# Performance work log

Measured on AMD Instinct MI355X. Metric: run time of the kernel, lower is better.

Reference implementation:

```python
import jax, jax.numpy as jnp
import numpy as np

IMG = 224                      # hardcoded image_size in apply_mask
K = int(0.25 * IMG * IMG)      # 12544 pixels masked per sample


def setup_inputs() -> dict:
    key = jax.random.key(0)
    k1, k2 = jax.random.split(key)
    B = 256
    data = jax.random.normal(k1, (B, IMG, IMG, 3), dtype=jnp.float32)
    # |gradients| flattened over (H, W, C) -> length IMG*IMG*3, nonnegative
    line_grad = jax.random.uniform(k2, (B, IMG * IMG * 3), dtype=jnp.float32)
    return {"data": data, "line_grad": line_grad}


def _mask_one(d, g):
    # d: [IMG, IMG, 3], g: [IMG*IMG*3]
    _, idx = jax.lax.top_k(g, K)              # flat indices into (H,W,C)
    reduced = jnp.mod(idx, IMG * IMG)         # fold channel offset -> spatial
    rows = reduced // IMG
    cols = reduced % IMG
    # scatter zeros across all 3 channels at the selected pixels
    return d.at[rows, cols].set(0.0)


def reference(data, line_grad):
    # vectorized_map over the batch -> vmap
    return jax.vmap(_mask_one)(data, line_grad)
```

## Files before the change

### kernel.cpp

```cpp
#include <hip/hip_runtime.h>

#define IMG    224
#define NPIX   (IMG * IMG)
#define NELEM  (NPIX * 3)
#define KSEL   12544
#define NBINS  4096
#define MAXCAND 2048
#define NMASKW (NPIX / 32)
#define NVEC   (NELEM / 4)
#define BLOCK  1024

__global__ __launch_bounds__(BLOCK) void masked_model_kernel(
    const float* __restrict__ data,
    const float* __restrict__ grad,
    float* __restrict__ out)
{
    const int b   = blockIdx.x;
    const int tid = threadIdx.x;

    const float* g = grad + (size_t)b * NELEM;
    const float* d = data + (size_t)b * NELEM;
    float*       o = out  + (size_t)b * NELEM;

    __shared__ unsigned int hist[NBINS];
    __shared__ unsigned int suffixP[BLOCK + 1];
    __shared__ unsigned int mask[NMASKW];
    __shared__ unsigned int candkey[MAXCAND];
    __shared__ unsigned int candidx[MAXCAND];
    __shared__ unsigned int candcnt;
    __shared__ int sB1;
    __shared__ unsigned int sR;

    for (int i = tid; i < NBINS; i += BLOCK) hist[i] = 0u;
    for (int i = tid; i < NMASKW; i += BLOCK) mask[i] = 0u;
    if (tid == 0) { candcnt = 0u; suffixP[BLOCK] = 0u; }
    __syncthreads();

    const float4* g4 = (const float4*)g;
    for (int i = tid; i < NVEC; i += BLOCK) {
        float4 v = g4[i];
        int b0 = min((int)(v.x * 4096.0f), NBINS - 1);
        int b1 = min((int)(v.y * 4096.0f), NBINS - 1);
        int b2 = min((int)(v.z * 4096.0f), NBINS - 1);
        int b3 = min((int)(v.w * 4096.0f), NBINS - 1);
        atomicAdd(&hist[b0], 1u);
        atomicAdd(&hist[b1], 1u);
        atomicAdd(&hist[b2], 1u);
        atomicAdd(&hist[b3], 1u);
    }
    __syncthreads();

    {
        unsigned int s = hist[4 * tid] + hist[4 * tid + 1]
                       + hist[4 * tid + 2] + hist[4 * tid + 3];
        suffixP[tid] = s;
        __syncthreads();
        for (int off = 1; off < BLOCK; off <<= 1) {
            unsigned int v = suffixP[tid];
            if (tid + off < BLOCK) v += suffixP[tid + off];
            __syncthreads();
            suffixP[tid] = v;
            __syncthreads();
        }
    }

    {
        unsigned int a  = suffixP[tid];
        unsigned int nx = suffixP[tid + 1];
        if (a >= KSEL && nx < KSEL) {
            unsigned int cum = nx;
            for (int i = 3; i >= 0; --i) {
                unsigned int h = hist[4 * tid + i];
                cum += h;
                if (cum >= KSEL) {
                    sB1 = 4 * tid + i;
                    sR  = KSEL - (cum - h);
                    break;
                }
            }
        }
    }
    __syncthreads();

    {
        const int B1 = sB1;
        for (int i = tid; i < NVEC; i += BLOCK) {
            float4 v = g4[i];
            int base = 4 * i;
            float vv[4] = {v.x, v.y, v.z, v.w};
            #pragma unroll
            for (int c = 0; c < 4; ++c) {
                int bin = min((int)(vv[c] * 4096.0f), NBINS - 1);
                if (bin > B1) {
                    int idx = base + c;
                    int p = idx % NPIX;
                    atomicOr(&mask[p >> 5], 1u << (p & 31));
                } else if (bin == B1) {
                    unsigned int c2 = atomicAdd(&candcnt, 1u);
                    if (c2 < MAXCAND) {
                        candkey[c2] = __float_as_uint(vv[c]);
                        candidx[c2] = (unsigned int)(base + c);
                    }
                }
            }
        }
    }
    __syncthreads();

    {
        unsigned int n = candcnt < MAXCAND ? candcnt : MAXCAND;
        unsigned int r = sR;
        for (unsigned int j = tid; j < n; j += BLOCK) {
            unsigned int kj = candkey[j];
            unsigned int ij = candidx[j];
            unsigned int rank = 0;
            for (unsigned int i = 0; i < n; ++i) {
                unsigned int ki = candkey[i];
                rank += (ki > kj) || (ki == kj && candidx[i] < ij);
            }
            if (rank < r) {
                int p = (int)(ij % NPIX);
                atomicOr(&mask[p >> 5], 1u << (p & 31));
            }
        }
    }
    __syncthreads();

    {
        const float4* d4 = (const float4*)d;
        float4*       o4 = (float4*)o;
        for (int i = tid; i < NVEC; i += BLOCK) {
            float4 v = d4[i];
            int e = 4 * i;
            int p0 = e / 3, p1 = (e + 1) / 3, p2 = (e + 2) / 3, p3 = (e + 3) / 3;
            if ((mask[p0 >> 5] >> (p0 & 31)) & 1u) v.x = 0.0f;
            if ((mask[p1 >> 5] >> (p1 & 31)) & 1u) v.y = 0.0f;
            if ((mask[p2 >> 5] >> (p2 & 31)) & 1u) v.z = 0.0f;
            if ((mask[p3 >> 5] >> (p3 & 31)) & 1u) v.w = 0.0f;
            o4[i] = v;
        }
    }
}

extern "C" void kernel_launch(void* const* d_in, const int* in_sizes, int n_in,
                              void* d_out, int out_size, void* d_ws, size_t ws_size,
                              hipStream_t stream) {
    const float* data = (const float*)d_in[0];
    const float* grad = (const float*)d_in[1];
    float* out = (float*)d_out;

    const int B = in_sizes[0] / NELEM;
    masked_model_kernel<<<B, BLOCK, 0, stream>>>(data, grad, out);
}
```

Before: 386.2 us.

## Split per-sample top-k masking into multi-kernel pipeline with more blocks per sample

Replaces the single block-per-sample kernel with four kernels: a chunked histogram built in workspace, a wave-shuffle suffix scan to find the threshold bin, a per-pixel-chunk apply kernel that checks all three channel planes per pixel and collects boundary candidates, and a small tie-resolution kernel that zeroes the extra pixels in the output. The aim is more parallelism than 256 large blocks allow, and removing the serial Hillis-Steele scan. In exchange it adds extra launches, a memset and reads the gradients twice from global memory. The candidate cap drops to 512, and the old kernel is used only when the workspace is too small.

New measurement: 397.3 us. 1.03x slower.

```diff
diff --git a/kernel.cpp b/kernel.cpp
--- a/kernel.cpp
+++ b/kernel.cpp
@@ -5,9 +5,185 @@
 #define NELEM  (NPIX * 3)
 #define KSEL   12544
 #define NBINS  4096
+#define NVEC4  (NELEM / 4)
+
+#define K1_CHUNKS 4
+#define K1_BLOCK  256
+#define K1_V4     (NVEC4 / K1_CHUNKS)
+
+#define CH        8
+#define PIX_PER   (NPIX / CH)
+#define QUADS_PER (PIX_PER / 4)
+#define MWORDS    (PIX_PER / 32)
+#define EV4_PER   (PIX_PER * 3 / 4)
+
+#define CAP 512
+
+__global__ __launch_bounds__(K1_BLOCK) void k1_hist(
+    const float* __restrict__ grad, unsigned int* __restrict__ hist)
+{
+    const int s     = blockIdx.x >> 2;
+    const int chunk = blockIdx.x & 3;
+    const float4* g4 = (const float4*)(grad + (size_t)s * NELEM);
+
+    __shared__ unsigned int h[NBINS];
+    for (int i = threadIdx.x; i < NBINS; i += K1_BLOCK) h[i] = 0u;
+    __syncthreads();
+
+    const int beg = chunk * K1_V4, end = beg + K1_V4;
+    for (int i = beg + threadIdx.x; i < end; i += K1_BLOCK) {
+        float4 v = g4[i];
+        atomicAdd(&h[min((int)(v.x * 4096.0f), NBINS - 1)], 1u);
+        atomicAdd(&h[min((int)(v.y * 4096.0f), NBINS - 1)], 1u);
+        atomicAdd(&h[min((int)(v.z * 4096.0f), NBINS - 1)], 1u);
+        atomicAdd(&h[min((int)(v.w * 4096.0f), NBINS - 1)], 1u);
+    }
+    __syncthreads();
+
+    unsigned int* gh = hist + (size_t)s * NBINS;
+    for (int i = threadIdx.x; i < NBINS; i += K1_BLOCK)
+        if (h[i]) atomicAdd(&gh[i], h[i]);
+}
+
+__global__ __launch_bounds__(1024) void k2_scan(
+    const unsigned int* __restrict__ hist,
+    uint2* __restrict__ thr, unsigned int* __restrict__ candcnt)
+{
+    const int s   = blockIdx.x;
+    const int tid = threadIdx.x;
+    const unsigned int* h = hist + (size_t)s * NBINS;
+
+    unsigned int h0 = h[4 * tid], h1 = h[4 * tid + 1];
+    unsigned int h2 = h[4 * tid + 2], h3 = h[4 * tid + 3];
+    const unsigned int gsum = h0 + h1 + h2 + h3;
+
+    const int lane = tid & 63, w = tid >> 6;
+    unsigned int v = gsum;
+    #pragma unroll
+    for (int off = 1; off < 64; off <<= 1) {
+        unsigned int u = __shfl_down(v, off, 64);
+        if (lane + off < 64) v += u;
+    }
+    __shared__ unsigned int wtot[16];
+    if (lane == 0) wtot[w] = v;
+    __syncthreads();
+    unsigned int tail = 0;
+    for (int i = w + 1; i < 16; ++i) tail += wtot[i];
+
+    const unsigned int suffix     = v + tail;
+    const unsigned int suffixNext = suffix - gsum;
+
+    if (suffix >= KSEL && suffixNext < KSEL) {
+        unsigned int cum = suffixNext;
+        unsigned int hh[4] = {h0, h1, h2, h3};
+        for (int i = 3; i >= 0; --i) {
+            cum += hh[i];
+            if (cum >= KSEL) {
+                thr[s] = make_uint2((unsigned)(4 * tid + i),
+                                    (unsigned)(KSEL - (cum - hh[i])));
+                break;
+            }
+        }
+    }
+    if (tid == 0) candcnt[s] = 0u;
+}
+
+__global__ __launch_bounds__(256) void k3_apply(
+    const float* __restrict__ data, const float* __restrict__ grad,
+    const uint2* __restrict__ thr,
+    unsigned int* __restrict__ candcnt,
+    unsigned int* __restrict__ candkey, unsigned int* __restrict__ candidx,
+    float* __restrict__ out)
+{
+    const int s     = blockIdx.x >> 3;
+    const int chunk = blockIdx.x & 7;
+    const int p0    = chunk * PIX_PER;
+
+    const uint2 t  = thr[s];
+    const float t0 = (float)t.x * (1.0f / 4096.0f);
+    const float t1 = (float)(t.x + 1) * (1.0f / 4096.0f);
+
+    __shared__ unsigned int mask[MWORDS];
+    for (int i = threadIdx.x; i < MWORDS; i += 256) mask[i] = 0u;
+    __syncthreads();
+
+    const float4* g4 = (const float4*)(grad + (size_t)s * NELEM);
+    unsigned int* ck = candkey + (size_t)s * CAP;
+    unsigned int* ci = candidx + (size_t)s * CAP;
+
+    for (int q = threadIdx.x; q < QUADS_PER; q += 256) {
+        const int p = p0 + 4 * q;
+        float4 a = g4[p >> 2];
+        float4 b = g4[(p + NPIX) >> 2];
+        float4 c = g4[(p + 2 * NPIX) >> 2];
+        float av[4] = {a.x, a.y, a.z, a.w};
+        float bv[4] = {b.x, b.y, b.z, b.w};
+        float cv[4] = {c.x, c.y, c.z, c.w};
+        unsigned int m = 0;
+        #pragma unroll
+        for (int j = 0; j < 4; ++j) {
+            if ((av[j] >= t1) || (bv[j] >= t1) || (cv[j] >= t1)) m |= (1u << j);
+            if (av[j] >= t0 && av[j] < t1) {
+                unsigned int cc = atomicAdd(&candcnt[s], 1u);
+                if (cc < CAP) { ck[cc] = __float_as_uint(av[j]); ci[cc] = (unsigned)(p + j); }
+            }
+            if (bv[j] >= t0 && bv[j] < t1) {
+                unsigned int cc = atomicAdd(&candcnt[s], 1u);
+                if (cc < CAP) { ck[cc] = __float_as_uint(bv[j]); ci[cc] = (unsigned)(NPIX + p + j); }
+            }
+            if (cv[j] >= t0 && cv[j] < t1) {
+                unsigned int cc = atomicAdd(&candcnt[s], 1u);
+                if (cc < CAP) { ck[cc] = __float_as_uint(cv[j]); ci[cc] = (unsigned)(2 * NPIX + p + j); }
+            }
+        }
+        if (m) atomicOr(&mask[q >> 3], m << ((4 * q) & 31));
+    }
+    __syncthreads();
+
+    const float4* d4 = (const float4*)(data + (size_t)s * NELEM + (size_t)3 * p0);
+    float4*       o4 = (float4*)(out  + (size_t)s * NELEM + (size_t)3 * p0);
+    for (int i = threadIdx.x; i < EV4_PER; i += 256) {
+        float4 v = d4[i];
+        const int e = 4 * i;
+        const int lp0 = e / 3, lp1 = (e + 1) / 3, lp2 = (e + 2) / 3, lp3 = (e + 3) / 3;
+        if ((mask[lp0 >> 5] >> (lp0 & 31)) & 1u) v.x = 0.0f;
+        if ((mask[lp1 >> 5] >> (lp1 & 31)) & 1u) v.y = 0.0f;
+        if ((mask[lp2 >> 5] >> (lp2 & 31)) & 1u) v.z = 0.0f;
+        if ((mask[lp3 >> 5] >> (lp3 & 31)) & 1u) v.w = 0.0f;
+        o4[i] = v;
+    }
+}
+
+__global__ __launch_bounds__(64) void k4_ties(
+    const uint2* __restrict__ thr, const unsigned int* __restrict__ candcnt,
+    const unsigned int* __restrict__ candkey, const unsigned int* __restrict__ candidx,
+    float* __restrict__ out)
+{
+    const int s = blockIdx.x;
+    const unsigned int n = min(candcnt[s], (unsigned int)CAP);
+    const unsigned int r = thr[s].y;
+    const unsigned int* ck = candkey + (size_t)s * CAP;
+    const unsigned int* ci = candidx + (size_t)s * CAP;
+
+    __shared__ unsigned int k_[CAP], i_[CAP];
+    for (unsigned int i = threadIdx.x; i < n; i += 64) { k_[i] = ck[i]; i_[i] = ci[i]; }
+    __syncthreads();
+
+    float* o = out + (size_t)s * NELEM;
+    for (unsigned int j = threadIdx.x; j < n; j += 64) {
+        const unsigned int kj = k_[j], ij = i_[j];
+        unsigned int rank = 0;
+        for (unsigned int i = 0; i < n; ++i)
+            rank += (k_[i] > kj) || (k_[i] == kj && i_[i] < ij);
+        if (rank < r) {
+            const int p = (int)(ij % NPIX);
+            o[3 * p] = 0.0f; o[3 * p + 1] = 0.0f; o[3 * p + 2] = 0.0f;
+        }
+    }
+}
+
 #define MAXCAND 2048
 #define NMASKW (NPIX / 32)
-#define NVEC   (NELEM / 4)
 #define BLOCK  1024
 
 __global__ __launch_bounds__(BLOCK) void masked_model_kernel(
@@ -37,23 +213,19 @@
     __syncthreads();
 
     const float4* g4 = (const float4*)g;
-    for (int i = tid; i < NVEC; i += BLOCK) {
+    for (int i = tid; i < NVEC4; i += BLOCK) {
         float4 v = g4[i];
-        int b0 = min((int)(v.x * 4096.0f), NBINS - 1);
-        int b1 = min((int)(v.y * 4096.0f), NBINS - 1);
-        int b2 = min((int)(v.z * 4096.0f), NBINS - 1);
-        int b3 = min((int)(v.w * 4096.0f), NBINS - 1);
-        atomicAdd(&hist[b0], 1u);
-        atomicAdd(&hist[b1], 1u);
-        atomicAdd(&hist[b2], 1u);
-        atomicAdd(&hist[b3], 1u);
-    }
-    __syncthreads();
-
-    {
-        unsigned int s = hist[4 * tid] + hist[4 * tid + 1]
-                       + hist[4 * tid + 2] + hist[4 * tid + 3];
-        suffixP[tid] = s;
+        atomicAdd(&hist[min((int)(v.x * 4096.0f), NBINS - 1)], 1u);
+        atomicAdd(&hist[min((int)(v.y * 4096.0f), NBINS - 1)], 1u);
+        atomicAdd(&hist[min((int)(v.z * 4096.0f), NBINS - 1)], 1u);
+        atomicAdd(&hist[min((int)(v.w * 4096.0f), NBINS - 1)], 1u);
+    }
+    __syncthreads();
+
+    {
+        unsigned int sv = hist[4 * tid] + hist[4 * tid + 1]
+                        + hist[4 * tid + 2] + hist[4 * tid + 3];
+        suffixP[tid] = sv;
         __syncthreads();
         for (int off = 1; off < BLOCK; off <<= 1) {
             unsigned int v = suffixP[tid];
@@ -63,7 +235,6 @@
             __syncthreads();
         }
     }
-
     {
         unsigned int a  = suffixP[tid];
         unsigned int nx = suffixP[tid + 1];
@@ -72,11 +243,7 @@
             for (int i = 3; i >= 0; --i) {
                 unsigned int h = hist[4 * tid + i];
                 cum += h;
-                if (cum >= KSEL) {
-                    sB1 = 4 * tid + i;
-                    sR  = KSEL - (cum - h);
-                    break;
-                }
+                if (cum >= KSEL) { sB1 = 4 * tid + i; sR = KSEL - (cum - h); break; }
             }
         }
     }
@@ -84,7 +251,7 @@
 
     {
         const int B1 = sB1;
-        for (int i = tid; i < NVEC; i += BLOCK) {
+        for (int i = tid; i < NVEC4; i += BLOCK) {
             float4 v = g4[i];
             int base = 4 * i;
             float vv[4] = {v.x, v.y, v.z, v.w};
@@ -92,8 +259,7 @@
             for (int c = 0; c < 4; ++c) {
                 int bin = min((int)(vv[c] * 4096.0f), NBINS - 1);
                 if (bin > B1) {
-                    int idx = base + c;
-                    int p = idx % NPIX;
+                    int p = (base + c) % NPIX;
                     atomicOr(&mask[p >> 5], 1u << (p & 31));
                 } else if (bin == B1) {
                     unsigned int c2 = atomicAdd(&candcnt, 1u);
@@ -129,7 +295,7 @@
     {
         const float4* d4 = (const float4*)d;
         float4*       o4 = (float4*)o;
-        for (int i = tid; i < NVEC; i += BLOCK) {
+        for (int i = tid; i < NVEC4; i += BLOCK) {
             float4 v = d4[i];
             int e = 4 * i;
             int p0 = e / 3, p1 = (e + 1) / 3, p2 = (e + 2) / 3, p3 = (e + 3) / 3;
@@ -150,5 +316,28 @@
     float* out = (float*)d_out;
 
     const int B = in_sizes[0] / NELEM;
-    masked_model_kernel<<<B, BLOCK, 0, stream>>>(data, grad, out);
-}
+
+    const size_t histB = (size_t)B * NBINS * sizeof(unsigned int);
+    const size_t thrB  = (size_t)B * sizeof(uint2);
+    const size_t cntB  = (size_t)B * sizeof(unsigned int);
+    const size_t cntPad = (cntB + 7) & ~(size_t)7;
+    const size_t keyB  = (size_t)B * CAP * sizeof(unsigned int);
+
+    char* p = (char*)d_ws;
+    unsigned int* hist = (unsigned int*)p;  p += histB;
+    uint2*        thr  = (uint2*)p;         p += thrB;
+    unsigned int* cnt  = (unsigned int*)p;  p += cntPad;
+    unsigned int* ckey = (unsigned int*)p;  p += keyB;
+    unsigned int* cidx = (unsigned int*)p;  p += keyB;
+    const size_t need = (size_t)(p - (char*)d_ws);
+
+    if (ws_size >= need) {
+        hipMemsetAsync(hist, 0, histB, stream);
+        k1_hist<<<B * K1_CHUNKS, K1_BLOCK, 0, stream>>>(grad, hist);
+        k2_scan<<<B, 1024, 0, stream>>>(hist, thr, cnt);
+        k3_apply<<<B * CH, 256, 0, stream>>>(data, grad, thr, cnt, ckey, cidx, out);
+        k4_ties<<<B, 64, 0, stream>>>(thr, cnt, ckey, cidx, out);
+    } else {
+        masked_model_kernel<<<B, BLOCK, 0, stream>>>(data, grad, out);
+    }
+}
```
